# Kernel tuning notes

Hardware: AMD Instinct MI355X
Metric: run time of the kernel (lower is better)

The kernel has to match this reference:

```python
import jax, jax.numpy as jnp
import numpy as np

H = 128
NH = 8
HD = H // NH  # 16
TANH_ALPHA = 10.0
LN_EPS = 1e-5


def _layer_norm(x, g, b):
    mu = jnp.mean(x, axis=-1, keepdims=True)
    var = jnp.mean((x - mu) ** 2, axis=-1, keepdims=True)
    return (x - mu) / jnp.sqrt(var + LN_EPS) * g + b


def setup_inputs() -> dict:
    key = jax.random.key(0)
    ks = jax.random.split(key, 24)
    B, N = 1024, 500

    def p(k, shape):
        return jax.random.normal(k, shape, dtype=jnp.float32) * 0.05

    inp = {
        "node_embeddings": jax.random.normal(ks[0], (B, N, H), jnp.float32),
        "graph_embeddings": jax.random.normal(ks[1], (B, H), jnp.float32),
        "first_node": jax.random.randint(ks[2], (B,), 0, N, jnp.int32),
        "current_node": jax.random.randint(ks[3], (B,), 0, N, jnp.int32),
        "mask": jax.random.randint(ks[4], (B, N), 0, 2, jnp.int32),
        # linear_first: Linear(384, 128)
        "W_first": p(ks[5], (H, 3 * H)),
        "b_first": p(ks[6], (H,)),
        # ln1 / ln2
        "g1": jnp.ones((H,), jnp.float32),
        "beta1": jnp.zeros((H,), jnp.float32),
        "g2": jnp.ones((H,), jnp.float32),
        "beta2": jnp.zeros((H,), jnp.float32),
        # LSTM(128,128) single layer, gate order i,f,g,o
        "W_ih": p(ks[7], (4 * H, H)),
        "W_hh": p(ks[8], (4 * H, H)),
        "b_ih": p(ks[9], (4 * H,)),
        "b_hh": p(ks[10], (4 * H,)),
        # attention / output projections (no bias)
        "Wq": p(ks[11], (H, H)),
        "Wk": p(ks[12], (H, H)),
        "Wv": p(ks[13], (H, H)),
        "Wproj": p(ks[14], (H, H)),
        # logitk: Linear(128,128) with bias
        "Wlk": p(ks[15], (H, H)),
        "blk": p(ks[16], (H,)),
    }
    return inp


def reference(node_embeddings, graph_embeddings, W_first, b_first, g1, beta1,
              W_ih, W_hh, b_ih, b_hh, g2, beta2, Wq, Wk, Wv, Wproj, Wlk, blk,
              first_node, current_node, mask):
    B, N, _ = node_embeddings.shape
    dt = node_embeddings.dtype

    # build_cache: K/V/logitK projections of all node embeddings
    ck = node_embeddings @ Wk.T                # [B,N,128]
    cv = node_embeddings @ Wv.T                # [B,N,128]
    lk = node_embeddings @ Wlk.T + blk         # [B,N,128]

    # context construction
    bidx = jnp.arange(B)
    first_emb = node_embeddings[bidx, first_node]    # [B,128]
    cur_emb = node_embeddings[bidx, current_node]    # [B,128]
    context = jnp.concatenate([graph_embeddings, first_emb, cur_emb], axis=1)
    context = _layer_norm(context @ W_first.T + b_first, g1, beta1)

    # single LSTM step from zero state (build_cache resets h,c to 0)
    gates = context @ W_ih.T + b_ih + b_hh           # h_prev = 0 -> no W_hh term
    i, f, g, o = jnp.split(gates, 4, axis=-1)
    c = jax.nn.sigmoid(i) * jnp.tanh(g)              # c_prev = 0
    h = jax.nn.sigmoid(o) * jnp.tanh(c)
    ctx = _layer_norm(h, g2, beta2)

    # multi-head single-query attention; note (e h) split: head is the FAST dim
    q = (ctx @ Wq.T).reshape(B, HD, NH).transpose(0, 2, 1)       # [B,h,e]
    k = ck.reshape(B, N, HD, NH).transpose(0, 3, 1, 2)           # [B,h,N,e]
    v = cv.reshape(B, N, HD, NH).transpose(0, 3, 1, 2)           # [B,h,N,e]
    maskf = mask.astype(dt)
    scores = jnp.einsum('bhe,bhne->bhn', q, k) / np.sqrt(HD) + maskf[:, None, :]
    att = jax.nn.softmax(scores, axis=-1)
    oh = jnp.einsum('bhn,bhne->bhe', att, v)                     # [B,h,e]
    att_out = oh.reshape(B, H)                                   # (h e): h slow, e fast

    context_emb = att_out @ Wproj.T                              # [B,128]
    comp = jnp.einsum('be,bne->bn', lk, context_emb[:, None, :].squeeze(1)[:, :][None].squeeze(0) if False else context_emb) if False else jnp.einsum('bne,be->bn', lk, context_emb)
    comp = comp / np.sqrt(H)
    comp = TANH_ALPHA * jnp.tanh(comp)
    out = jnp.where(mask == 1, -jnp.inf, comp)
    return out
```

## Files before the change

### kernel.cpp

```cpp
#include <hip/hip_runtime.h>
#include <math.h>

#define NBATCH 1024
#define NNODE  500
#define HDIM   128
#define NHEAD  8
#define G1K    4
#define RSQRT_H 0.08838834764831845f
#define MASK_NEG (-1e30f)

typedef __attribute__((ext_vector_type(8))) short  short8;
typedef __attribute__((ext_vector_type(4))) float  f32x4;

__device__ __forceinline__ short bftr(float f) {
    return (short)(__float_as_uint(f) >> 16);
}

template<int G>
__device__ __forceinline__ void block_ln(float (&x)[G], const float* __restrict__ gw,
                                         const float* __restrict__ bw,
                                         int t, int lane, int wv, float (*wpart)[G])
{
    float s[G];
    #pragma unroll
    for (int g = 0; g < G; ++g) s[g] = x[g];
    #pragma unroll
    for (int off = 32; off >= 1; off >>= 1) {
        #pragma unroll
        for (int g = 0; g < G; ++g) s[g] += __shfl_xor(s[g], off, 64);
    }
    if (lane == 0) {
        #pragma unroll
        for (int g = 0; g < G; ++g) wpart[wv][g] = s[g];
    }
    __syncthreads();
    float mu[G];
    #pragma unroll
    for (int g = 0; g < G; ++g) mu[g] = (wpart[0][g] + wpart[1][g]) * (1.f/128.f);
    __syncthreads();
    #pragma unroll
    for (int g = 0; g < G; ++g) { float d = x[g] - mu[g]; s[g] = d * d; }
    #pragma unroll
    for (int off = 32; off >= 1; off >>= 1) {
        #pragma unroll
        for (int g = 0; g < G; ++g) s[g] += __shfl_xor(s[g], off, 64);
    }
    if (lane == 0) {
        #pragma unroll
        for (int g = 0; g < G; ++g) wpart[wv][g] = s[g];
    }
    __syncthreads();
    float gv = gw[t], bv = bw[t];
    #pragma unroll
    for (int g = 0; g < G; ++g) {
        float var = (wpart[0][g] + wpart[1][g]) * (1.f/128.f);
        x[g] = (x[g] - mu[g]) / sqrtf(var + 1e-5f) * gv + bv;
    }
    __syncthreads();
}

__global__ __launch_bounds__(128) void k1_context(
    const float* __restrict__ node, const float* __restrict__ graph,
    const int* __restrict__ firstn, const int* __restrict__ curn,
    const float* __restrict__ W_first, const float* __restrict__ b_first,
    const float* __restrict__ g1, const float* __restrict__ beta1,
    const float* __restrict__ W_ih, const float* __restrict__ b_ih,
    const float* __restrict__ b_hh, const float* __restrict__ g2,
    const float* __restrict__ beta2, const float* __restrict__ Wq,
    const float* __restrict__ Wk, float* __restrict__ qW_out)
{
    const int t = threadIdx.x;
    const int lane = t & 63, wv = t >> 6;
    const int b0 = blockIdx.x * G1K;
    __shared__ __align__(16) float ctx[G1K][384];
    __shared__ __align__(16) float bufB[G1K][128];
    __shared__ float wpart[2][G1K];

    #pragma unroll
    for (int g = 0; g < G1K; ++g) {
        int b = b0 + g;
        ctx[g][t]       = graph[b*HDIM + t];
        ctx[g][128 + t] = node[((size_t)b*NNODE + firstn[b])*HDIM + t];
        ctx[g][256 + t] = node[((size_t)b*NNODE + curn[b])*HDIM + t];
    }
    __syncthreads();

    float x[G1K];
    {
        const float4* Wf4 = (const float4*)W_first;
        float bf = b_first[t];
        #pragma unroll
        for (int g = 0; g < G1K; ++g) x[g] = bf;
        for (int j4 = 0; j4 < 96; ++j4) {
            float4 w = Wf4[t*96 + j4];
            #pragma unroll
            for (int g = 0; g < G1K; ++g) {
                float4 c = ((const float4*)ctx[g])[j4];
                x[g] += c.x*w.x + c.y*w.y + c.z*w.z + c.w*w.w;
            }
        }
    }
    block_ln<G1K>(x, g1, beta1, t, lane, wv, wpart);

    #pragma unroll
    for (int g = 0; g < G1K; ++g) bufB[g][t] = x[g];
    __syncthreads();

    float gi[G1K], gg[G1K], go[G1K];
    {
        const float4* Wih4 = (const float4*)W_ih;
        float bi = b_ih[t]       + b_hh[t];
        float bg = b_ih[256 + t] + b_hh[256 + t];
        float bo = b_ih[384 + t] + b_hh[384 + t];
        #pragma unroll
        for (int g = 0; g < G1K; ++g) { gi[g] = bi; gg[g] = bg; go[g] = bo; }
        for (int j4 = 0; j4 < 32; ++j4) {
            float4 wi = Wih4[(size_t)t*32 + j4];
            float4 wg = Wih4[(size_t)(256 + t)*32 + j4];
            float4 wo = Wih4[(size_t)(384 + t)*32 + j4];
            #pragma unroll
            for (int g = 0; g < G1K; ++g) {
                float4 v = ((const float4*)bufB[g])[j4];
                gi[g] += v.x*wi.x + v.y*wi.y + v.z*wi.z + v.w*wi.w;
                gg[g] += v.x*wg.x + v.y*wg.y + v.z*wg.z + v.w*wg.w;
                go[g] += v.x*wo.x + v.y*wo.y + v.z*wo.z + v.w*wo.w;
            }
        }
    }
    #pragma unroll
    for (int g = 0; g < G1K; ++g) {
        float ig = 1.f / (1.f + expf(-gi[g]));
        float cc = ig * tanhf(gg[g]);
        float og = 1.f / (1.f + expf(-go[g]));
        x[g] = og * tanhf(cc);
    }
    block_ln<G1K>(x, g2, beta2, t, lane, wv, wpart);

    #pragma unroll
    for (int g = 0; g < G1K; ++g) bufB[g][t] = x[g];
    __syncthreads();

    float q8[G1K];
    #pragma unroll
    for (int g = 0; g < G1K; ++g) q8[g] = 0.f;
    {
        const float4* Wq4 = (const float4*)Wq;
        for (int j4 = 0; j4 < 32; ++j4) {
            float4 w = Wq4[t*32 + j4];
            #pragma unroll
            for (int g = 0; g < G1K; ++g) {
                float4 v = ((const float4*)bufB[g])[j4];
                q8[g] += v.x*w.x + v.y*w.y + v.z*w.z + v.w*w.w;
            }
        }
    }
    __syncthreads();
    #pragma unroll
    for (int g = 0; g < G1K; ++g) bufB[g][t] = q8[g];
    __syncthreads();

    for (int h = 0; h < NHEAD; ++h) {
        float a[G1K];
        #pragma unroll
        for (int g = 0; g < G1K; ++g) a[g] = 0.f;
        for (int e = 0; e < 16; ++e) {
            float w = Wk[(e*8 + h)*HDIM + t];
            #pragma unroll
            for (int g = 0; g < G1K; ++g) a[g] += bufB[g][e*8 + h] * w;
        }
        #pragma unroll
        for (int g = 0; g < G1K; ++g)
            qW_out[((size_t)(b0 + g)*NHEAD + h)*HDIM + t] = 0.25f * a[g];
    }
}

__global__ __launch_bounds__(256, 4) void k2_fused(
    const float* __restrict__ node, const int* __restrict__ mask,
    const float* __restrict__ qW, const float* __restrict__ Wv,
    const float* __restrict__ Wproj, const float* __restrict__ Wlk,
    const float* __restrict__ blk_, float* __restrict__ wce_out,
    float* __restrict__ bias_out)
{
    const int b = blockIdx.x, tid = threadIdx.x;
    const int lane = tid & 63, w = tid >> 6;
    const int h = lane & 15;
    const bool hok = (h < NHEAD);
    const int g16 = lane >> 4;
    const int koff = g16 << 3;

    __shared__ __align__(16) float s_p[NHEAD*NNODE];
    __shared__ float s_red[4][8];
    __shared__ float s_m[8], s_l[8];
    __shared__ __align__(16) float s_an[NHEAD*HDIM];
    __shared__ __align__(16) float s_ao[HDIM], s_ce[HDIM];
    __shared__ __align__(16) float s_part[8][HDIM];

    const float* nodeb = node + (size_t)b*NNODE*HDIM;

    {
        short8 bfr[4];
        {
            const float* qrow = qW + ((size_t)b*NHEAD + (hok ? h : 0))*HDIM;
            #pragma unroll
            for (int kk = 0; kk < 4; ++kk) {
                short8 f = (short8)0;
                if (hok) {
                    float4 w0 = *(const float4*)(qrow + kk*32 + koff);
                    float4 w1 = *(const float4*)(qrow + kk*32 + koff + 4);
                    f[0]=bftr(w0.x); f[1]=bftr(w0.y); f[2]=bftr(w0.z); f[3]=bftr(w0.w);
                    f[4]=bftr(w1.x); f[5]=bftr(w1.y); f[6]=bftr(w1.z); f[7]=bftr(w1.w);
                }
                bfr[kk] = f;
            }
        }

        float4 Ra[8], Rb[8];
        auto loadit = [&](float4* R, int it) {
            const int rl = it*64 + w*16 + (lane & 15);
            if (rl < NNODE) {
                const float* nrow = nodeb + (size_t)rl*HDIM;
                #pragma unroll
                for (int kk = 0; kk < 4; ++kk) {
                    R[kk*2]   = *(const float4*)(nrow + kk*32 + koff);
                    R[kk*2+1] = *(const float4*)(nrow + kk*32 + koff + 4);
                }
            } else {
                #pragma unroll
                for (int i = 0; i < 8; ++i) R[i] = make_float4(0.f,0.f,0.f,0.f);
            }
        };
        auto computeit = [&](const float4* R, int it) {
            f32x4 acc = {0.f, 0.f, 0.f, 0.f};
            #pragma unroll
            for (int kk = 0; kk < 4; ++kk) {
                float4 v0 = R[kk*2], v1 = R[kk*2+1];
                short8 afr;
                afr[0]=bftr(v0.x); afr[1]=bftr(v0.y); afr[2]=bftr(v0.z); afr[3]=bftr(v0.w);
                afr[4]=bftr(v1.x); afr[5]=bftr(v1.y); afr[6]=bftr(v1.z); afr[7]=bftr(v1.w);
                acc = __builtin_amdgcn_mfma_f32_16x16x32_bf16(afr, bfr[kk], acc, 0, 0, 0);
            }
            if (hok) {
                #pragma unroll
                for (int j = 0; j < 4; ++j) {
                    int r = it*64 + w*16 + g16*4 + j;
                    if (r < NNODE) s_p[h*NNODE + r] = acc[j];
                }
            }
        };

        loadit(Ra, 0);
        loadit(Rb, 1);
        #pragma unroll
        for (int it = 0; it < 8; ++it) {
            float4* cur = (it & 1) ? Rb : Ra;
            computeit(cur, it);
            if (it + 2 < 8) loadit(cur, it + 2);
        }
    }
    __syncthreads();

    const int* maskb = mask + (size_t)b*NNODE;
    {
        float mx[8];
        #pragma unroll
        for (int hh = 0; hh < 8; ++hh) mx[hh] = -INFINITY;
        for (int r = tid; r < NNODE; r += 256) {
            float mf = (float)maskb[r];
            #pragma unroll
            for (int hh = 0; hh < 8; ++hh) {
                float v = s_p[hh*NNODE + r] + mf;
                s_p[hh*NNODE + r] = v;
                mx[hh] = fmaxf(mx[hh], v);
            }
        }
        #pragma unroll
        for (int off = 1; off <= 32; off <<= 1) {
            #pragma unroll
            for (int hh = 0; hh < 8; ++hh) mx[hh] = fmaxf(mx[hh], __shfl_xor(mx[hh], off, 64));
        }
        if (lane == 0) {
            #pragma unroll
            for (int hh = 0; hh < 8; ++hh) s_red[w][hh] = mx[hh];
        }
        __syncthreads();
        if (tid < 8)
            s_m[tid] = fmaxf(fmaxf(s_red[0][tid], s_red[1][tid]),
                             fmaxf(s_red[2][tid], s_red[3][tid]));
        __syncthreads();
        float ls[8];
        #pragma unroll
        for (int hh = 0; hh < 8; ++hh) ls[hh] = 0.f;
        for (int r = tid; r < NNODE; r += 256) {
            #pragma unroll
            for (int hh = 0; hh < 8; ++hh) {
                float p = __expf(s_p[hh*NNODE + r] - s_m[hh]);
                s_p[hh*NNODE + r] = p;
                ls[hh] += p;
            }
        }
        #pragma unroll
        for (int off = 1; off <= 32; off <<= 1) {
            #pragma unroll
            for (int hh = 0; hh < 8; ++hh) ls[hh] += __shfl_xor(ls[hh], off, 64);
        }
        if (lane == 0) {
            #pragma unroll
            for (int hh = 0; hh < 8; ++hh) s_red[w][hh] = ls[hh];
        }
        __syncthreads();
        if (tid < 8)
            s_l[tid] = s_red[0][tid] + s_red[1][tid] + s_red[2][tid] + s_red[3][tid];
        __syncthreads();
    }

    {
        const int h2 = tid >> 5, d8 = tid & 31;
        f32x4 acc = {0.f, 0.f, 0.f, 0.f};
        const float4* nb4 = (const float4*)nodeb + d8;
        const float* prow = s_p + h2*NNODE;
        #pragma unroll 10
        for (int n = 0; n < NNODE; ++n) {
            float4 v = nb4[(size_t)n*32];
            float p = prow[n];
            acc[0] += p*v.x; acc[1] += p*v.y; acc[2] += p*v.z; acc[3] += p*v.w;
        }
        float inv = 1.f / s_l[h2];
        float4 o = make_float4(acc[0]*inv, acc[1]*inv, acc[2]*inv, acc[3]*inv);
        *(float4*)(s_an + h2*HDIM + d8*4) = o;
    }
    __syncthreads();

    {
        const int c = tid >> 1, half = tid & 1;
        const int hh = c >> 4, e = c & 15, row = e*8 + hh;
        const float4* wr = (const float4*)(Wv + (size_t)row*HDIM) + half*16;
        const float4* ar = (const float4*)(s_an + hh*HDIM) + half*16;
        float sum = 0.f;
        #pragma unroll
        for (int j = 0; j < 16; ++j) {
            float4 wv4 = wr[j], av = ar[j];
            sum += av.x*wv4.x + av.y*wv4.y + av.z*wv4.z + av.w*wv4.w;
        }
        sum += __shfl_xor(sum, 1, 64);
        if (half == 0) s_ao[c] = sum;
    }
    __syncthreads();
    {
        const int c = tid >> 1, half = tid & 1;
        const float4* wr = (const float4*)(Wproj + (size_t)c*HDIM) + half*16;
        const float4* ar = (const float4*)s_ao + half*16;
        float sum = 0.f;
        #pragma unroll
        for (int j = 0; j < 16; ++j) {
            float4 wv4 = wr[j], av = ar[j];
            sum += av.x*wv4.x + av.y*wv4.y + av.z*wv4.z + av.w*wv4.w;
        }
        sum += __shfl_xor(sum, 1, 64);
        if (half == 0) s_ce[c] = sum;
    }
    __syncthreads();
    {
        const int cg = tid >> 5, dq = tid & 31;
        float4 part = make_float4(0.f, 0.f, 0.f, 0.f);
        #pragma unroll
        for (int i = 0; i < 16; ++i) {
            int c = cg*16 + i;
            float v = s_ce[c];
            float4 wv4 = ((const float4*)(Wlk + (size_t)c*HDIM))[dq];
            part.x += v*wv4.x; part.y += v*wv4.y;
            part.z += v*wv4.z; part.w += v*wv4.w;
        }
        *(float4*)(s_part[cg] + dq*4) = part;
    }
    __syncthreads();
    if (tid < 32) {
        float4 tot = make_float4(0.f, 0.f, 0.f, 0.f);
        #pragma unroll
        for (int cg = 0; cg < 8; ++cg) {
            float4 v = *(float4*)(s_part[cg] + tid*4);
            tot.x += v.x; tot.y += v.y; tot.z += v.z; tot.w += v.w;
        }
        tot.x *= RSQRT_H; tot.y *= RSQRT_H; tot.z *= RSQRT_H; tot.w *= RSQRT_H;
        *(float4*)(wce_out + (size_t)b*HDIM + tid*4) = tot;
    }
    else if (tid >= 64 && tid < 128) {
        int c = tid - 64;
        float v = s_ce[c]*blk_[c] + s_ce[c+64]*blk_[c+64];
        #pragma unroll
        for (int off = 1; off <= 32; off <<= 1) v += __shfl_xor(v, off, 64);
        if (c == 0) bias_out[b] = v * RSQRT_H;
    }
}

__global__ __launch_bounds__(256) void k3_out(
    const float* __restrict__ node, const int* __restrict__ mask,
    const float* __restrict__ wce, const float* __restrict__ biasv,
    float* __restrict__ out)
{
    const int slot = (int)((blockIdx.x*256u + threadIdx.x) >> 5);
    const int q = threadIdx.x & 31;
    const int b = slot / NNODE;
    const float4 nv = *(const float4*)(node + (size_t)slot*HDIM + q*4);
    const float4 wv = *(const float4*)(wce + (size_t)b*HDIM + q*4);
    float p = nv.x*wv.x + nv.y*wv.y + nv.z*wv.z + nv.w*wv.w;
    #pragma unroll
    for (int off = 16; off >= 1; off >>= 1) p += __shfl_xor(p, off, 32);
    if (q == 0) {
        float v = 10.f * tanhf(p + biasv[b]);
        out[slot] = (mask[slot] == 1) ? MASK_NEG : v;
    }
}

extern "C" void kernel_launch(void* const* d_in, const int* in_sizes, int n_in,
                              void* d_out, int out_size, void* d_ws, size_t ws_size,
                              hipStream_t stream) {
    const float* node    = (const float*)d_in[0];
    const float* graph   = (const float*)d_in[1];
    const int*   firstn  = (const int*)d_in[2];
    const int*   curn    = (const int*)d_in[3];
    const int*   mask    = (const int*)d_in[4];
    const float* W_first = (const float*)d_in[5];
    const float* b_first = (const float*)d_in[6];
    const float* g1      = (const float*)d_in[7];
    const float* beta1   = (const float*)d_in[8];
    const float* g2      = (const float*)d_in[9];
    const float* beta2   = (const float*)d_in[10];
    const float* W_ih    = (const float*)d_in[11];
    const float* b_ih    = (const float*)d_in[13];
    const float* b_hh    = (const float*)d_in[14];
    const float* Wq      = (const float*)d_in[15];
    const float* Wk      = (const float*)d_in[16];
    const float* Wv      = (const float*)d_in[17];
    const float* Wproj   = (const float*)d_in[18];
    const float* Wlk     = (const float*)d_in[19];
    const float* blk     = (const float*)d_in[20];
    float* out = (float*)d_out;

    float* qW    = (float*)d_ws;
    float* wce   = qW + (size_t)NBATCH*NHEAD*HDIM;
    float* biasv = wce + (size_t)NBATCH*HDIM;

    k1_context<<<NBATCH/G1K, 128, 0, stream>>>(node, graph, firstn, curn,
        W_first, b_first, g1, beta1, W_ih, b_ih, b_hh, g2, beta2, Wq, Wk, qW);
    k2_fused<<<NBATCH, 256, 0, stream>>>(node, mask, qW, Wv, Wproj, Wlk, blk,
        wce, biasv);
    k3_out<<<(NBATCH*NNODE)/8, 256, 0, stream>>>(node, mask, wce, biasv, out);
}
```

Before: 220.8 us.

## Split attention over node halves with flash-style partial softmax merge kernel

The fused per-batch attention kernel becomes two kernels. The first runs two blocks per batch, each handling 250 nodes and writing a partial max, sum and unnormalised weighted value to workspace. The second merges the two halves with rescaling and then does the Wv, Wproj and Wlk projections. This doubles the block count and cuts shared memory per block to raise occupancy and parallelism, at the cost of an extra launch, a workspace round-trip, and dropping the register double-buffered load pipeline.

```diff
diff --git a/kernel.cpp b/kernel.cpp
--- a/kernel.cpp
+++ b/kernel.cpp
@@ -3,9 +3,11 @@
 
 #define NBATCH 1024
 #define NNODE  500
+#define HALFN  250
 #define HDIM   128
 #define NHEAD  8
 #define G1K    4
+#define PSTRIDE 1056
 #define RSQRT_H 0.08838834764831845f
 #define MASK_NEG (-1e30f)
 
@@ -174,28 +176,24 @@
     }
 }
 
-__global__ __launch_bounds__(256, 4) void k2_fused(
+__global__ __launch_bounds__(256, 8) void k2a_half(
     const float* __restrict__ node, const int* __restrict__ mask,
-    const float* __restrict__ qW, const float* __restrict__ Wv,
-    const float* __restrict__ Wproj, const float* __restrict__ Wlk,
-    const float* __restrict__ blk_, float* __restrict__ wce_out,
-    float* __restrict__ bias_out)
+    const float* __restrict__ qW, float* __restrict__ part)
 {
-    const int b = blockIdx.x, tid = threadIdx.x;
+    const int b = blockIdx.x >> 1;
+    const int s = blockIdx.x & 1;
+    const int tid = threadIdx.x;
     const int lane = tid & 63, w = tid >> 6;
     const int h = lane & 15;
     const bool hok = (h < NHEAD);
     const int g16 = lane >> 4;
     const int koff = g16 << 3;
 
-    __shared__ __align__(16) float s_p[NHEAD*NNODE];
+    __shared__ __align__(16) float s_p[NHEAD][252];
     __shared__ float s_red[4][8];
     __shared__ float s_m[8], s_l[8];
-    __shared__ __align__(16) float s_an[NHEAD*HDIM];
-    __shared__ __align__(16) float s_ao[HDIM], s_ce[HDIM];
-    __shared__ __align__(16) float s_part[8][HDIM];
-
-    const float* nodeb = node + (size_t)b*NNODE*HDIM;
+
+    const float* nodeb = node + ((size_t)b*NNODE + s*HALFN)*HDIM;
 
     {
         short8 bfr[4];
@@ -213,27 +211,26 @@
                 bfr[kk] = f;
             }
         }
-
-        float4 Ra[8], Rb[8];
-        auto loadit = [&](float4* R, int it) {
+        #pragma unroll
+        for (int it = 0; it < 4; ++it) {
             const int rl = it*64 + w*16 + (lane & 15);
-            if (rl < NNODE) {
-                const float* nrow = nodeb + (size_t)rl*HDIM;
+            const bool rok = (rl < HALFN);
+            const float* nrow = nodeb + (size_t)rl*HDIM;
+            float4 v[8];
+            if (rok) {
                 #pragma unroll
                 for (int kk = 0; kk < 4; ++kk) {
-                    R[kk*2]   = *(const float4*)(nrow + kk*32 + koff);
-                    R[kk*2+1] = *(const float4*)(nrow + kk*32 + koff + 4);
+                    v[kk*2]   = *(const float4*)(nrow + kk*32 + koff);
+                    v[kk*2+1] = *(const float4*)(nrow + kk*32 + koff + 4);
                 }
             } else {
                 #pragma unroll
-                for (int i = 0; i < 8; ++i) R[i] = make_float4(0.f,0.f,0.f,0.f);
-            }
-        };
-        auto computeit = [&](const float4* R, int it) {
+                for (int i = 0; i < 8; ++i) v[i] = make_float4(0.f,0.f,0.f,0.f);
+            }
             f32x4 acc = {0.f, 0.f, 0.f, 0.f};
             #pragma unroll
             for (int kk = 0; kk < 4; ++kk) {
-                float4 v0 = R[kk*2], v1 = R[kk*2+1];
+                float4 v0 = v[kk*2], v1 = v[kk*2+1];
                 short8 afr;
                 afr[0]=bftr(v0.x); afr[1]=bftr(v0.y); afr[2]=bftr(v0.z); afr[3]=bftr(v0.w);
                 afr[4]=bftr(v1.x); afr[5]=bftr(v1.y); afr[6]=bftr(v1.z); afr[7]=bftr(v1.w);
@@ -243,40 +240,32 @@
                 #pragma unroll
                 for (int j = 0; j < 4; ++j) {
                     int r = it*64 + w*16 + g16*4 + j;
-                    if (r < NNODE) s_p[h*NNODE + r] = acc[j];
+                    if (r < HALFN) s_p[h][r] = acc[j];
                 }
             }
-        };
-
-        loadit(Ra, 0);
-        loadit(Rb, 1);
-        #pragma unroll
-        for (int it = 0; it < 8; ++it) {
-            float4* cur = (it & 1) ? Rb : Ra;
-            computeit(cur, it);
-            if (it + 2 < 8) loadit(cur, it + 2);
-        }
-    }
-    __syncthreads();
-
-    const int* maskb = mask + (size_t)b*NNODE;
-    {
+        }
+    }
+    __syncthreads();
+
+    {
+        const int r = tid;
         float mx[8];
         #pragma unroll
         for (int hh = 0; hh < 8; ++hh) mx[hh] = -INFINITY;
-        for (int r = tid; r < NNODE; r += 256) {
-            float mf = (float)maskb[r];
+        if (r < HALFN) {
+            float mf = (float)mask[(size_t)b*NNODE + s*HALFN + r];
             #pragma unroll
             for (int hh = 0; hh < 8; ++hh) {
-                float v = s_p[hh*NNODE + r] + mf;
-                s_p[hh*NNODE + r] = v;
-                mx[hh] = fmaxf(mx[hh], v);
+                float v = s_p[hh][r] + mf;
+                s_p[hh][r] = v;
+                mx[hh] = v;
             }
         }
         #pragma unroll
         for (int off = 1; off <= 32; off <<= 1) {
             #pragma unroll
-            for (int hh = 0; hh < 8; ++hh) mx[hh] = fmaxf(mx[hh], __shfl_xor(mx[hh], off, 64));
+            for (int hh = 0; hh < 8; ++hh)
+                mx[hh] = fmaxf(mx[hh], __shfl_xor(mx[hh], off, 64));
         }
         if (lane == 0) {
             #pragma unroll
@@ -290,12 +279,12 @@
         float ls[8];
         #pragma unroll
         for (int hh = 0; hh < 8; ++hh) ls[hh] = 0.f;
-        for (int r = tid; r < NNODE; r += 256) {
+        if (r < HALFN) {
             #pragma unroll
             for (int hh = 0; hh < 8; ++hh) {
-                float p = __expf(s_p[hh*NNODE + r] - s_m[hh]);
-                s_p[hh*NNODE + r] = p;
-                ls[hh] += p;
+                float p = __expf(s_p[hh][r] - s_m[hh]);
+                s_p[hh][r] = p;
+                ls[hh] = p;
             }
         }
         #pragma unroll
@@ -317,16 +306,45 @@
         const int h2 = tid >> 5, d8 = tid & 31;
         f32x4 acc = {0.f, 0.f, 0.f, 0.f};
         const float4* nb4 = (const float4*)nodeb + d8;
-        const float* prow = s_p + h2*NNODE;
+        const float* prow = s_p[h2];
         #pragma unroll 10
-        for (int n = 0; n < NNODE; ++n) {
+        for (int n = 0; n < HALFN; ++n) {
             float4 v = nb4[(size_t)n*32];
             float p = prow[n];
             acc[0] += p*v.x; acc[1] += p*v.y; acc[2] += p*v.z; acc[3] += p*v.w;
         }
-        float inv = 1.f / s_l[h2];
-        float4 o = make_float4(acc[0]*inv, acc[1]*inv, acc[2]*inv, acc[3]*inv);
-        *(float4*)(s_an + h2*HDIM + d8*4) = o;
+        float* pbase = part + (size_t)blockIdx.x * PSTRIDE;
+        if (tid < 8) { pbase[tid] = s_m[tid]; pbase[8 + tid] = s_l[tid]; }
+        float4 o = make_float4(acc[0], acc[1], acc[2], acc[3]);
+        *(float4*)(pbase + 16 + h2*HDIM + d8*4) = o;
+    }
+}
+
+__global__ __launch_bounds__(256) void k2b_merge(
+    const float* __restrict__ part, const float* __restrict__ Wv,
+    const float* __restrict__ Wproj, const float* __restrict__ Wlk,
+    const float* __restrict__ blk_, float* __restrict__ wce_out,
+    float* __restrict__ bias_out)
+{
+    const int b = blockIdx.x, tid = threadIdx.x;
+    __shared__ __align__(16) float s_an[NHEAD*HDIM];
+    __shared__ __align__(16) float s_ao[HDIM], s_ce[HDIM];
+    __shared__ __align__(16) float s_part[8][HDIM];
+
+    {
+        const int h = tid >> 5, q = tid & 31;
+        const float* p0 = part + (size_t)(b*2)   * PSTRIDE;
+        const float* p1 = part + (size_t)(b*2+1) * PSTRIDE;
+        float m0 = p0[h], l0 = p0[8 + h];
+        float m1 = p1[h], l1 = p1[8 + h];
+        float gm = fmaxf(m0, m1);
+        float f0 = __expf(m0 - gm), f1 = __expf(m1 - gm);
+        float inv = 1.f / (l0*f0 + l1*f1);
+        float4 v0 = *(const float4*)(p0 + 16 + h*HDIM + q*4);
+        float4 v1 = *(const float4*)(p1 + 16 + h*HDIM + q*4);
+        float4 o = make_float4((v0.x*f0 + v1.x*f1)*inv, (v0.y*f0 + v1.y*f1)*inv,
+                               (v0.z*f0 + v1.z*f1)*inv, (v0.w*f0 + v1.w*f1)*inv);
+        *(float4*)(s_an + h*HDIM + q*4) = o;
     }
     __syncthreads();
 
@@ -361,16 +379,16 @@
     __syncthreads();
     {
         const int cg = tid >> 5, dq = tid & 31;
-        float4 part = make_float4(0.f, 0.f, 0.f, 0.f);
+        float4 pt = make_float4(0.f, 0.f, 0.f, 0.f);
         #pragma unroll
         for (int i = 0; i < 16; ++i) {
             int c = cg*16 + i;
             float v = s_ce[c];
             float4 wv4 = ((const float4*)(Wlk + (size_t)c*HDIM))[dq];
-            part.x += v*wv4.x; part.y += v*wv4.y;
-            part.z += v*wv4.z; part.w += v*wv4.w;
-        }
-        *(float4*)(s_part[cg] + dq*4) = part;
+            pt.x += v*wv4.x; pt.y += v*wv4.y;
+            pt.z += v*wv4.z; pt.w += v*wv4.w;
+        }
+        *(float4*)(s_part[cg] + dq*4) = pt;
     }
     __syncthreads();
     if (tid < 32) {
@@ -439,10 +457,12 @@
     float* qW    = (float*)d_ws;
     float* wce   = qW + (size_t)NBATCH*NHEAD*HDIM;
     float* biasv = wce + (size_t)NBATCH*HDIM;
+    float* part  = biasv + NBATCH;
 
     k1_context<<<NBATCH/G1K, 128, 0, stream>>>(node, graph, firstn, curn,
         W_first, b_first, g1, beta1, W_ih, b_ih, b_hh, g2, beta2, Wq, Wk, qW);
-    k2_fused<<<NBATCH, 256, 0, stream>>>(node, mask, qW, Wv, Wproj, Wlk, blk,
+    k2a_half<<<NBATCH*2, 256, 0, stream>>>(node, mask, qW, part);
+    k2b_merge<<<NBATCH, 256, 0, stream>>>(part, Wv, Wproj, Wlk, blk,
         wce, biasv);
     k3_out<<<(NBATCH*NNODE)/8, 256, 0, stream>>>(node, mask, wce, biasv, out);
 }
```

Result: no change. 221.7 us (+0.4%).
